# Optimization experiments

Measured on AMD Instinct MI355X. Metric: run time of the kernel, lower is better.

The kernel has to match this reference:

```python
import jax, jax.numpy as jnp
import numpy as np

B_, N, C, H = 8192, 49, 192, 6
HD = C // H
SCALE = HD ** -0.5


def setup_inputs() -> dict:
    key = jax.random.key(0)
    k0, k1, k2, k3 = jax.random.split(key, 4)
    x = jax.random.normal(k0, (B_, N, C), dtype=jnp.float32)
    mask = jax.random.randint(k1, (B_, N), 0, 2, dtype=jnp.int32)
    w_qkv = jax.random.normal(k2, (C, 3 * C), dtype=jnp.float32) * 0.02
    b_qkv = jnp.zeros((3 * C,), dtype=jnp.float32)
    w_proj = jax.random.normal(k3, (C, C), dtype=jnp.float32) * 0.02
    b_proj = jnp.zeros((C,), dtype=jnp.float32)
    return {"x": x, "mask": mask, "w_qkv": w_qkv, "b_qkv": b_qkv,
            "w_proj": w_proj, "b_proj": b_proj}


def reference(x, mask, w_qkv, b_qkv, w_proj, b_proj):
    # qkv projection: [B_, N, 3C] -> [3, B_, H, N, HD]
    qkv = (x @ w_qkv + b_qkv).reshape(B_, N, 3, H, HD).transpose(2, 0, 3, 1, 4)
    q, k, v = qkv[0], qkv[1], qkv[2]
    # scaled QK^T: [B_, H, N, N]
    attn = jnp.einsum('bhnd,bhmd->bhnm', q, k) * SCALE
    # additive key mask: mask==0 positions get -inf
    attn = jnp.where(mask[:, None, None, :] == 0, -jnp.inf, attn)
    p = jax.nn.softmax(attn, axis=-1)  # dropout p=0 -> identity
    out = jnp.einsum('bhnm,bhmd->bhnd', p, v)  # AV
    out = out.transpose(0, 2, 1, 3).reshape(B_, N, C)
    return out @ w_proj + b_proj
```

## Files before the change

### kernel.cpp

```cpp
#include <hip/hip_runtime.h>


typedef __attribute__((ext_vector_type(8))) short short8;
typedef __attribute__((ext_vector_type(4))) float f32x4;

#define SCALE 0.17677669529663687f

__device__ __forceinline__ unsigned short f2bf(float x) {
    union { float f; unsigned int i; } v; v.f = x;
    return (unsigned short)((v.i + 0x7FFFu + ((v.i >> 16) & 1u)) >> 16);
}

__device__ __forceinline__ unsigned int pkbf(float lo, float hi) {
    unsigned int r;
    asm("v_cvt_pk_bf16_f32 %0, %1, %2" : "=v"(r) : "v"(lo), "v"(hi));
    return r;
}

__device__ __forceinline__ int swz64(int row, int col) {
    return row * 64 + ((((col >> 3) ^ (row & 7)) << 3) | (col & 7));
}

__device__ __forceinline__ short8 xpose(f32x4 tlo, f32x4 thi, int srcA, bool hi) {
    unsigned int pl0 = pkbf(tlo[0], tlo[1]);
    unsigned int pl1 = pkbf(tlo[2], tlo[3]);
    unsigned int ph0 = pkbf(thi[0], thi[1]);
    unsigned int ph1 = pkbf(thi[2], thi[3]);
    unsigned int a0 = (unsigned int)__shfl((int)pl0, srcA);
    unsigned int b0 = (unsigned int)__shfl((int)ph0, srcA);
    unsigned int a1 = (unsigned int)__shfl((int)pl1, srcA);
    unsigned int b1 = (unsigned int)__shfl((int)ph1, srcA);
    unsigned int a2 = (unsigned int)__shfl((int)pl0, srcA + 16);
    unsigned int b2 = (unsigned int)__shfl((int)ph0, srcA + 16);
    unsigned int a3 = (unsigned int)__shfl((int)pl1, srcA + 16);
    unsigned int b3 = (unsigned int)__shfl((int)ph1, srcA + 16);
    union { short8 s8; unsigned int u[4]; } f;
    f.u[0] = hi ? b0 : a0;
    f.u[1] = hi ? b1 : a1;
    f.u[2] = hi ? b2 : a2;
    f.u[3] = hi ? b3 : a3;
    return f.s8;
}

__global__ void repack_kernel(const float* __restrict__ wqkv,
                              const float* __restrict__ wproj,
                              unsigned short* __restrict__ wq_pack,
                              unsigned short* __restrict__ wp_pack) {
    int idx = blockIdx.x * 256 + threadIdx.x;
    if (idx < 6 * 576 * 32) {
        int kk  = idx & 31;
        int col = (idx >> 5) % 576;
        int kt  = idx / (576 * 32);
        wq_pack[idx] = f2bf(wqkv[(kt * 32 + kk) * 576 + col]);
    } else {
        int j = idx - 6 * 576 * 32;
        if (j < 6 * 192 * 32) {
            int kk  = j & 31;
            int col = (j >> 5) % 192;
            int kt  = j / (192 * 32);
            wp_pack[j] = f2bf(wproj[(kt * 32 + kk) * 192 + col]);
        }
    }
}

__global__ __launch_bounds__(384)
void win_attn_kernel(const float* __restrict__ x,
                     const int* __restrict__ mask,
                     const float* __restrict__ bqkv,
                     const float* __restrict__ bproj,
                     const unsigned short* __restrict__ wq,
                     const unsigned short* __restrict__ wpj,
                     float* __restrict__ out) {
    __shared__ __align__(16) unsigned short region[25088];
    __shared__ __align__(16) float mbias[64];

    const int b    = blockIdx.x;
    const int tid  = threadIdx.x;
    const int lane = tid & 63;
    const int h    = tid >> 6;
    const int quad = lane >> 4;
    const int l16  = lane & 15;

    const float* xb = x + (size_t)b * 9408;
    for (int i4 = tid; i4 < 2352; i4 += 384) {
        int flat = i4 * 4;
        int n = flat / 192, c = flat % 192;
        float4 v = *(const float4*)(const void*)&xb[flat];
        uint2 pk;
        pk.x = pkbf(v.x, v.y);
        pk.y = pkbf(v.z, v.w);
        *(uint2*)(void*)&region[n * 200 + c] = pk;
    }
    if (tid < 375) {
        uint4 z = {0u, 0u, 0u, 0u};
        *(uint4*)(void*)&region[9800 + tid * 8] = z;
    }
    if (tid < 64)
        mbias[tid] = (tid < 49 && mask[b * 49 + tid] != 0) ? 0.0f : -1e30f;
    __syncthreads();

    const int  srcA = ((lane & 16) << 1) | l16;
    const bool hiq  = (lane & 32) != 0;

    int colb[6];
    #pragma unroll
    for (int t = 0; t < 6; ++t) colb[t] = (t >> 1) * 192 + h * 32 + (t & 1) * 16;

    short8 qf[4], kf[4];
    {
        f32x4 acc[4][4];
        #pragma unroll
        for (int t = 0; t < 4; ++t)
            #pragma unroll
            for (int mt = 0; mt < 4; ++mt)
                acc[t][mt] = (f32x4){0.f, 0.f, 0.f, 0.f};

        #pragma unroll
        for (int kt = 0; kt < 6; ++kt) {
            short8 af[4];
            #pragma unroll
            for (int mt = 0; mt < 4; ++mt)
                af[mt] = *(const short8*)(const void*)
                         &region[(mt * 16 + l16) * 200 + kt * 32 + quad * 8];
            #pragma unroll
            for (int t = 0; t < 4; ++t) {
                short8 bw = *(const short8*)(const void*)
                            &wq[(size_t)(kt * 576 + colb[t] + l16) * 32 + quad * 8];
                #pragma unroll
                for (int mt = 0; mt < 4; ++mt)
                    acc[t][mt] = __builtin_amdgcn_mfma_f32_16x16x32_bf16(
                                     bw, af[mt], acc[t][mt], 0, 0, 0);
            }
        }
        #pragma unroll
        for (int t = 0; t < 4; ++t) {
            f32x4 bq = *(const f32x4*)(const void*)&bqkv[colb[t] + quad * 4];
            #pragma unroll
            for (int nt = 0; nt < 4; ++nt)
                #pragma unroll
                for (int r = 0; r < 4; ++r)
                    acc[t][nt][r] += bq[r];
        }
        #pragma unroll
        for (int nt = 0; nt < 4; ++nt) {
            qf[nt] = xpose(acc[0][nt], acc[1][nt], srcA, hiq);
            kf[nt] = xpose(acc[2][nt], acc[3][nt], srcA, hiq);
        }
    }

    unsigned short* vtb = &region[12800 + h * 2048];
    {
        f32x4 accv[2][4];
        #pragma unroll
        for (int t = 0; t < 2; ++t)
            #pragma unroll
            for (int mt = 0; mt < 4; ++mt)
                accv[t][mt] = (f32x4){0.f, 0.f, 0.f, 0.f};

        #pragma unroll
        for (int kt = 0; kt < 6; ++kt) {
            short8 af[4];
            #pragma unroll
            for (int mt = 0; mt < 4; ++mt)
                af[mt] = *(const short8*)(const void*)
                         &region[(mt * 16 + l16) * 200 + kt * 32 + quad * 8];
            #pragma unroll
            for (int t = 0; t < 2; ++t) {
                short8 bw = *(const short8*)(const void*)
                            &wq[(size_t)(kt * 576 + colb[4 + t] + l16) * 32 + quad * 8];
                #pragma unroll
                for (int mt = 0; mt < 4; ++mt)
                    accv[t][mt] = __builtin_amdgcn_mfma_f32_16x16x32_bf16(
                                      af[mt], bw, accv[t][mt], 0, 0, 0);
            }
        }
        #pragma unroll
        for (int t = 0; t < 2; ++t) {
            float bv = bqkv[colb[4 + t] + l16];
            #pragma unroll
            for (int mt = 0; mt < 4; ++mt) {
                int d = t * 16 + l16;
                uint2 pk;
                pk.x = pkbf(accv[t][mt][0] + bv, accv[t][mt][1] + bv);
                pk.y = pkbf(accv[t][mt][2] + bv, accv[t][mt][3] + bv);
                *(uint2*)(void*)&vtb[swz64(d, mt * 16 + quad * 4)] = pk;
            }
        }
    }

    f32x4 mb4[4];
    #pragma unroll
    for (int mt = 0; mt < 4; ++mt)
        mb4[mt] = *(const f32x4*)(const void*)&mbias[mt * 16 + quad * 4];

    short8 ap[4][2];
    #pragma unroll
    for (int nt = 0; nt < 4; ++nt) {
        f32x4 sr[4];
        #pragma unroll
        for (int mt = 0; mt < 4; ++mt) {
            sr[mt] = (f32x4){0.f, 0.f, 0.f, 0.f};
            sr[mt] = __builtin_amdgcn_mfma_f32_16x16x32_bf16(
                         kf[mt], qf[nt], sr[mt], 0, 0, 0);
        }
        float pm[4];
        #pragma unroll
        for (int mt = 0; mt < 4; ++mt) {
            #pragma unroll
            for (int r = 0; r < 4; ++r)
                sr[mt][r] = sr[mt][r] * SCALE + mb4[mt][r];
            pm[mt] = fmaxf(fmaxf(sr[mt][0], sr[mt][1]),
                           fmaxf(sr[mt][2], sr[mt][3]));
        }
        float mx = fmaxf(fmaxf(pm[0], pm[1]), fmaxf(pm[2], pm[3]));
        mx = fmaxf(mx, __shfl_xor(mx, 16));
        mx = fmaxf(mx, __shfl_xor(mx, 32));
        float ps[4];
        #pragma unroll
        for (int mt = 0; mt < 4; ++mt) {
            #pragma unroll
            for (int r = 0; r < 4; ++r)
                sr[mt][r] = __expf(sr[mt][r] - mx);
            ps[mt] = (sr[mt][0] + sr[mt][1]) + (sr[mt][2] + sr[mt][3]);
        }
        float sum = (ps[0] + ps[1]) + (ps[2] + ps[3]);
        sum += __shfl_xor(sum, 16);
        sum += __shfl_xor(sum, 32);
        float inv = 1.0f / sum;
        #pragma unroll
        for (int mt = 0; mt < 4; ++mt)
            #pragma unroll
            for (int r = 0; r < 4; ++r)
                sr[mt][r] *= inv;
        ap[nt][0] = xpose(sr[0], sr[1], srcA, hiq);
        ap[nt][1] = xpose(sr[2], sr[3], srcA, hiq);
    }

    f32x4 o[4][2];
    #pragma unroll
    for (int mo = 0; mo < 4; ++mo)
        #pragma unroll
        for (int dt = 0; dt < 2; ++dt)
            o[mo][dt] = (f32x4){0.f, 0.f, 0.f, 0.f};

    #pragma unroll
    for (int kt = 0; kt < 2; ++kt) {
        short8 bvv[2];
        #pragma unroll
        for (int dt = 0; dt < 2; ++dt)
            bvv[dt] = *(const short8*)(const void*)
                      &vtb[swz64(dt * 16 + l16, kt * 32 + quad * 8)];
        #pragma unroll
        for (int mo = 0; mo < 4; ++mo)
            #pragma unroll
            for (int dt = 0; dt < 2; ++dt)
                o[mo][dt] = __builtin_amdgcn_mfma_f32_16x16x32_bf16(
                                ap[mo][kt], bvv[dt], o[mo][dt], 0, 0, 0);
    }

    __syncthreads();
    #pragma unroll
    for (int dt = 0; dt < 2; ++dt)
        #pragma unroll
        for (int mt = 0; mt < 4; ++mt)
            #pragma unroll
            for (int r = 0; r < 4; ++r)
                region[(mt * 16 + quad * 4 + r) * 200 + h * 32 + dt * 16 + l16]
                    = f2bf(o[mt][dt][r]);
    __syncthreads();

    f32x4 po[2][4];
    #pragma unroll
    for (int nt = 0; nt < 2; ++nt)
        #pragma unroll
        for (int mt = 0; mt < 4; ++mt)
            po[nt][mt] = (f32x4){0.f, 0.f, 0.f, 0.f};

    #pragma unroll
    for (int kt = 0; kt < 6; ++kt) {
        short8 ao[4];
        #pragma unroll
        for (int mt = 0; mt < 4; ++mt)
            ao[mt] = *(const short8*)(const void*)
                     &region[(mt * 16 + l16) * 200 + kt * 32 + quad * 8];
        #pragma unroll
        for (int nt = 0; nt < 2; ++nt) {
            int col = h * 32 + nt * 16 + l16;
            short8 bw = *(const short8*)(const void*)
                        &wpj[(size_t)(kt * 192 + col) * 32 + quad * 8];
            #pragma unroll
            for (int mt = 0; mt < 4; ++mt)
                po[nt][mt] = __builtin_amdgcn_mfma_f32_16x16x32_bf16(
                                 ao[mt], bw, po[nt][mt], 0, 0, 0);
        }
    }

    #pragma unroll
    for (int nt = 0; nt < 2; ++nt) {
        int col = h * 32 + nt * 16 + l16;
        float bv = bproj[col];
        #pragma unroll
        for (int mt = 0; mt < 4; ++mt)
            #pragma unroll
            for (int r = 0; r < 4; ++r) {
                int row = mt * 16 + quad * 4 + r;
                if (row < 49)
                    out[(size_t)b * 9408 + row * 192 + col] = po[nt][mt][r] + bv;
            }
    }
}

extern "C" void kernel_launch(void* const* d_in, const int* in_sizes, int n_in,
                              void* d_out, int out_size, void* d_ws, size_t ws_size,
                              hipStream_t stream) {
    const float* x      = (const float*)d_in[0];
    const int*   mask   = (const int*)d_in[1];
    const float* w_qkv  = (const float*)d_in[2];
    const float* b_qkv  = (const float*)d_in[3];
    const float* w_proj = (const float*)d_in[4];
    const float* b_proj = (const float*)d_in[5];
    float*       out    = (float*)d_out;

    unsigned short* wq_pack = (unsigned short*)d_ws;
    unsigned short* wp_pack = wq_pack + 110592;

    repack_kernel<<<(110592 + 36864 + 255) / 256, 256, 0, stream>>>(
        w_qkv, w_proj, wq_pack, wp_pack);
    win_attn_kernel<<<8192, 384, 0, stream>>>(x, mask, b_qkv, b_proj,
                                              wq_pack, wp_pack, out);
}
```

Before: 848.7 us.

## Make blocks persistent over eight windows with double-buffered prefetch of next window

Each block now handles eight consecutive windows instead of one. The next window's x and mask are loaded into registers at the start of each iteration and written to a second shared buffer after the attention step, so global load latency overlaps with compute. Shared memory grows (two x buffers plus per-head V tiles), and the grid shrinks from 8192 to 1024 blocks. The fewer, larger blocks may lower occupancy and weaken load balance across CUs.

```diff
diff --git a/kernel.cpp b/kernel.cpp
--- a/kernel.cpp
+++ b/kernel.cpp
@@ -5,6 +5,7 @@
 typedef __attribute__((ext_vector_type(4))) float f32x4;
 
 #define SCALE 0.17677669529663687f
+#define WPB   8
 
 __device__ __forceinline__ unsigned short f2bf(float x) {
     union { float f; unsigned int i; } v; v.f = x;
@@ -71,33 +72,16 @@
                      const unsigned short* __restrict__ wq,
                      const unsigned short* __restrict__ wpj,
                      float* __restrict__ out) {
-    __shared__ __align__(16) unsigned short region[25088];
-    __shared__ __align__(16) float mbias[64];
-
-    const int b    = blockIdx.x;
+    __shared__ __align__(16) unsigned short xbuf[2][12800];
+    __shared__ __align__(16) unsigned short vtl[6][2048];
+    __shared__ __align__(16) float mbias[2][64];
+
     const int tid  = threadIdx.x;
     const int lane = tid & 63;
     const int h    = tid >> 6;
     const int quad = lane >> 4;
     const int l16  = lane & 15;
-
-    const float* xb = x + (size_t)b * 9408;
-    for (int i4 = tid; i4 < 2352; i4 += 384) {
-        int flat = i4 * 4;
-        int n = flat / 192, c = flat % 192;
-        float4 v = *(const float4*)(const void*)&xb[flat];
-        uint2 pk;
-        pk.x = pkbf(v.x, v.y);
-        pk.y = pkbf(v.z, v.w);
-        *(uint2*)(void*)&region[n * 200 + c] = pk;
-    }
-    if (tid < 375) {
-        uint4 z = {0u, 0u, 0u, 0u};
-        *(uint4*)(void*)&region[9800 + tid * 8] = z;
-    }
-    if (tid < 64)
-        mbias[tid] = (tid < 49 && mask[b * 49 + tid] != 0) ? 0.0f : -1e30f;
-    __syncthreads();
+    const int b0   = blockIdx.x * WPB;
 
     const int  srcA = ((lane & 16) << 1) | l16;
     const bool hiq  = (lane & 32) != 0;
@@ -106,207 +90,282 @@
     #pragma unroll
     for (int t = 0; t < 6; ++t) colb[t] = (t >> 1) * 192 + h * 32 + (t & 1) * 16;
 
-    short8 qf[4], kf[4];
+    unsigned short* vtb = &vtl[h][0];
+
     {
-        f32x4 acc[4][4];
-        #pragma unroll
-        for (int t = 0; t < 4; ++t)
-            #pragma unroll
-            for (int mt = 0; mt < 4; ++mt)
-                acc[t][mt] = (f32x4){0.f, 0.f, 0.f, 0.f};
+        const float* xb = x + (size_t)b0 * 9408;
+        for (int i4 = tid; i4 < 2352; i4 += 384) {
+            int flat = i4 * 4;
+            int n = flat / 192, c = flat % 192;
+            float4 v = *(const float4*)(const void*)&xb[flat];
+            uint2 pk;
+            pk.x = pkbf(v.x, v.y);
+            pk.y = pkbf(v.z, v.w);
+            *(uint2*)(void*)&xbuf[0][n * 200 + c] = pk;
+        }
+        if (tid < 375) {
+            uint4 z = {0u, 0u, 0u, 0u};
+            *(uint4*)(void*)&xbuf[0][9800 + tid * 8] = z;
+        }
+        if (tid < 64)
+            mbias[0][tid] = (tid < 49 && mask[b0 * 49 + tid] != 0) ? 0.0f
+                                                                   : -1e30f;
+    }
+    __syncthreads();
+
+    int cur = 0;
+    for (int wi = 0; wi < WPB; ++wi, cur ^= 1) {
+        const int b = b0 + wi;
+        const bool more = (wi + 1 < WPB);
+
+        float4 st[6];
+        float4 st6 = {0.f, 0.f, 0.f, 0.f};
+        int mv = 0;
+        if (more) {
+            const float* xn = x + (size_t)(b + 1) * 9408;
+            #pragma unroll
+            for (int k = 0; k < 6; ++k)
+                st[k] = *(const float4*)(const void*)&xn[(tid + k * 384) * 4];
+            if (tid < 48)
+                st6 = *(const float4*)(const void*)&xn[(2304 + tid) * 4];
+            if (tid < 49)
+                mv = mask[(b + 1) * 49 + tid];
+        }
+
+        unsigned short* rg  = &xbuf[cur][0];
+        float*          mbp = &mbias[cur][0];
+
+        short8 qf[4], kf[4];
+        {
+            f32x4 acc[4][4];
+            #pragma unroll
+            for (int t = 0; t < 4; ++t)
+                #pragma unroll
+                for (int mt = 0; mt < 4; ++mt)
+                    acc[t][mt] = (f32x4){0.f, 0.f, 0.f, 0.f};
+
+            #pragma unroll
+            for (int kt = 0; kt < 6; ++kt) {
+                short8 af[4];
+                #pragma unroll
+                for (int mt = 0; mt < 4; ++mt)
+                    af[mt] = *(const short8*)(const void*)
+                             &rg[(mt * 16 + l16) * 200 + kt * 32 + quad * 8];
+                #pragma unroll
+                for (int t = 0; t < 4; ++t) {
+                    short8 bw = *(const short8*)(const void*)
+                                &wq[(size_t)(kt * 576 + colb[t] + l16) * 32 + quad * 8];
+                    #pragma unroll
+                    for (int mt = 0; mt < 4; ++mt)
+                        acc[t][mt] = __builtin_amdgcn_mfma_f32_16x16x32_bf16(
+                                         bw, af[mt], acc[t][mt], 0, 0, 0);
+                }
+            }
+            #pragma unroll
+            for (int t = 0; t < 4; ++t) {
+                f32x4 bq = *(const f32x4*)(const void*)&bqkv[colb[t] + quad * 4];
+                #pragma unroll
+                for (int nt = 0; nt < 4; ++nt)
+                    #pragma unroll
+                    for (int r = 0; r < 4; ++r)
+                        acc[t][nt][r] += bq[r];
+            }
+            #pragma unroll
+            for (int nt = 0; nt < 4; ++nt) {
+                qf[nt] = xpose(acc[0][nt], acc[1][nt], srcA, hiq);
+                kf[nt] = xpose(acc[2][nt], acc[3][nt], srcA, hiq);
+            }
+        }
+
+        {
+            f32x4 accv[2][4];
+            #pragma unroll
+            for (int t = 0; t < 2; ++t)
+                #pragma unroll
+                for (int mt = 0; mt < 4; ++mt)
+                    accv[t][mt] = (f32x4){0.f, 0.f, 0.f, 0.f};
+
+            #pragma unroll
+            for (int kt = 0; kt < 6; ++kt) {
+                short8 af[4];
+                #pragma unroll
+                for (int mt = 0; mt < 4; ++mt)
+                    af[mt] = *(const short8*)(const void*)
+                             &rg[(mt * 16 + l16) * 200 + kt * 32 + quad * 8];
+                #pragma unroll
+                for (int t = 0; t < 2; ++t) {
+                    short8 bw = *(const short8*)(const void*)
+                                &wq[(size_t)(kt * 576 + colb[4 + t] + l16) * 32 + quad * 8];
+                    #pragma unroll
+                    for (int mt = 0; mt < 4; ++mt)
+                        accv[t][mt] = __builtin_amdgcn_mfma_f32_16x16x32_bf16(
+                                          af[mt], bw, accv[t][mt], 0, 0, 0);
+                }
+            }
+            #pragma unroll
+            for (int t = 0; t < 2; ++t) {
+                float bv = bqkv[colb[4 + t] + l16];
+                #pragma unroll
+                for (int mt = 0; mt < 4; ++mt) {
+                    int d = t * 16 + l16;
+                    uint2 pk;
+                    pk.x = pkbf(accv[t][mt][0] + bv, accv[t][mt][1] + bv);
+                    pk.y = pkbf(accv[t][mt][2] + bv, accv[t][mt][3] + bv);
+                    *(uint2*)(void*)&vtb[swz64(d, mt * 16 + quad * 4)] = pk;
+                }
+            }
+        }
+
+        f32x4 mb4[4];
+        #pragma unroll
+        for (int mt = 0; mt < 4; ++mt)
+            mb4[mt] = *(const f32x4*)(const void*)&mbp[mt * 16 + quad * 4];
+
+        short8 ap[4][2];
+        #pragma unroll
+        for (int nt = 0; nt < 4; ++nt) {
+            f32x4 sr[4];
+            #pragma unroll
+            for (int mt = 0; mt < 4; ++mt) {
+                sr[mt] = (f32x4){0.f, 0.f, 0.f, 0.f};
+                sr[mt] = __builtin_amdgcn_mfma_f32_16x16x32_bf16(
+                             kf[mt], qf[nt], sr[mt], 0, 0, 0);
+            }
+            float pm[4];
+            #pragma unroll
+            for (int mt = 0; mt < 4; ++mt) {
+                #pragma unroll
+                for (int r = 0; r < 4; ++r)
+                    sr[mt][r] = sr[mt][r] * SCALE + mb4[mt][r];
+                pm[mt] = fmaxf(fmaxf(sr[mt][0], sr[mt][1]),
+                               fmaxf(sr[mt][2], sr[mt][3]));
+            }
+            float mx = fmaxf(fmaxf(pm[0], pm[1]), fmaxf(pm[2], pm[3]));
+            mx = fmaxf(mx, __shfl_xor(mx, 16));
+            mx = fmaxf(mx, __shfl_xor(mx, 32));
+            float ps[4];
+            #pragma unroll
+            for (int mt = 0; mt < 4; ++mt) {
+                #pragma unroll
+                for (int r = 0; r < 4; ++r)
+                    sr[mt][r] = __expf(sr[mt][r] - mx);
+                ps[mt] = (sr[mt][0] + sr[mt][1]) + (sr[mt][2] + sr[mt][3]);
+            }
+            float sum = (ps[0] + ps[1]) + (ps[2] + ps[3]);
+            sum += __shfl_xor(sum, 16);
+            sum += __shfl_xor(sum, 32);
+            float inv = 1.0f / sum;
+            #pragma unroll
+            for (int mt = 0; mt < 4; ++mt)
+                #pragma unroll
+                for (int r = 0; r < 4; ++r)
+                    sr[mt][r] *= inv;
+            ap[nt][0] = xpose(sr[0], sr[1], srcA, hiq);
+            ap[nt][1] = xpose(sr[2], sr[3], srcA, hiq);
+        }
+
+        f32x4 o[4][2];
+        #pragma unroll
+        for (int mo = 0; mo < 4; ++mo)
+            #pragma unroll
+            for (int dt = 0; dt < 2; ++dt)
+                o[mo][dt] = (f32x4){0.f, 0.f, 0.f, 0.f};
+
+        #pragma unroll
+        for (int kt = 0; kt < 2; ++kt) {
+            short8 bvv[2];
+            #pragma unroll
+            for (int dt = 0; dt < 2; ++dt)
+                bvv[dt] = *(const short8*)(const void*)
+                          &vtb[swz64(dt * 16 + l16, kt * 32 + quad * 8)];
+            #pragma unroll
+            for (int mo = 0; mo < 4; ++mo)
+                #pragma unroll
+                for (int dt = 0; dt < 2; ++dt)
+                    o[mo][dt] = __builtin_amdgcn_mfma_f32_16x16x32_bf16(
+                                    ap[mo][kt], bvv[dt], o[mo][dt], 0, 0, 0);
+        }
+
+        __syncthreads();
+
+        #pragma unroll
+        for (int dt = 0; dt < 2; ++dt)
+            #pragma unroll
+            for (int mt = 0; mt < 4; ++mt)
+                #pragma unroll
+                for (int r = 0; r < 4; ++r)
+                    rg[(mt * 16 + quad * 4 + r) * 200 + h * 32 + dt * 16 + l16]
+                        = f2bf(o[mt][dt][r]);
+
+        if (more) {
+            unsigned short* nb = &xbuf[cur ^ 1][0];
+            #pragma unroll
+            for (int k = 0; k < 6; ++k) {
+                int flat = (tid + k * 384) * 4;
+                int n = flat / 192, c = flat % 192;
+                uint2 pk;
+                pk.x = pkbf(st[k].x, st[k].y);
+                pk.y = pkbf(st[k].z, st[k].w);
+                *(uint2*)(void*)&nb[n * 200 + c] = pk;
+            }
+            if (tid < 48) {
+                int flat = (2304 + tid) * 4;
+                int n = flat / 192, c = flat % 192;
+                uint2 pk;
+                pk.x = pkbf(st6.x, st6.y);
+                pk.y = pkbf(st6.z, st6.w);
+                *(uint2*)(void*)&nb[n * 200 + c] = pk;
+            }
+            if (tid < 375) {
+                uint4 z = {0u, 0u, 0u, 0u};
+                *(uint4*)(void*)&nb[9800 + tid * 8] = z;
+            }
+            if (tid < 64)
+                mbias[cur ^ 1][tid] = (tid < 49 && mv != 0) ? 0.0f : -1e30f;
+        }
+
+        __syncthreads();
+
+        f32x4 po[2][4];
+        #pragma unroll
+        for (int nt = 0; nt < 2; ++nt)
+            #pragma unroll
+            for (int mt = 0; mt < 4; ++mt)
+                po[nt][mt] = (f32x4){0.f, 0.f, 0.f, 0.f};
 
         #pragma unroll
         for (int kt = 0; kt < 6; ++kt) {
-            short8 af[4];
-            #pragma unroll
-            for (int mt = 0; mt < 4; ++mt)
-                af[mt] = *(const short8*)(const void*)
-                         &region[(mt * 16 + l16) * 200 + kt * 32 + quad * 8];
-            #pragma unroll
-            for (int t = 0; t < 4; ++t) {
+            short8 ao[4];
+            #pragma unroll
+            for (int mt = 0; mt < 4; ++mt)
+                ao[mt] = *(const short8*)(const void*)
+                         &rg[(mt * 16 + l16) * 200 + kt * 32 + quad * 8];
+            #pragma unroll
+            for (int nt = 0; nt < 2; ++nt) {
+                int col = h * 32 + nt * 16 + l16;
                 short8 bw = *(const short8*)(const void*)
-                            &wq[(size_t)(kt * 576 + colb[t] + l16) * 32 + quad * 8];
-                #pragma unroll
-                for (int mt = 0; mt < 4; ++mt)
-                    acc[t][mt] = __builtin_amdgcn_mfma_f32_16x16x32_bf16(
-                                     bw, af[mt], acc[t][mt], 0, 0, 0);
-            }
-        }
-        #pragma unroll
-        for (int t = 0; t < 4; ++t) {
-            f32x4 bq = *(const f32x4*)(const void*)&bqkv[colb[t] + quad * 4];
-            #pragma unroll
-            for (int nt = 0; nt < 4; ++nt)
-                #pragma unroll
-                for (int r = 0; r < 4; ++r)
-                    acc[t][nt][r] += bq[r];
-        }
-        #pragma unroll
-        for (int nt = 0; nt < 4; ++nt) {
-            qf[nt] = xpose(acc[0][nt], acc[1][nt], srcA, hiq);
-            kf[nt] = xpose(acc[2][nt], acc[3][nt], srcA, hiq);
-        }
-    }
-
-    unsigned short* vtb = &region[12800 + h * 2048];
-    {
-        f32x4 accv[2][4];
-        #pragma unroll
-        for (int t = 0; t < 2; ++t)
-            #pragma unroll
-            for (int mt = 0; mt < 4; ++mt)
-                accv[t][mt] = (f32x4){0.f, 0.f, 0.f, 0.f};
-
-        #pragma unroll
-        for (int kt = 0; kt < 6; ++kt) {
-            short8 af[4];
-            #pragma unroll
-            for (int mt = 0; mt < 4; ++mt)
-                af[mt] = *(const short8*)(const void*)
-                         &region[(mt * 16 + l16) * 200 + kt * 32 + quad * 8];
-            #pragma unroll
-            for (int t = 0; t < 2; ++t) {
-                short8 bw = *(const short8*)(const void*)
-                            &wq[(size_t)(kt * 576 + colb[4 + t] + l16) * 32 + quad * 8];
-                #pragma unroll
-                for (int mt = 0; mt < 4; ++mt)
-                    accv[t][mt] = __builtin_amdgcn_mfma_f32_16x16x32_bf16(
-                                      af[mt], bw, accv[t][mt], 0, 0, 0);
-            }
-        }
-        #pragma unroll
-        for (int t = 0; t < 2; ++t) {
-            float bv = bqkv[colb[4 + t] + l16];
-            #pragma unroll
-            for (int mt = 0; mt < 4; ++mt) {
-                int d = t * 16 + l16;
-                uint2 pk;
-                pk.x = pkbf(accv[t][mt][0] + bv, accv[t][mt][1] + bv);
-                pk.y = pkbf(accv[t][mt][2] + bv, accv[t][mt][3] + bv);
-                *(uint2*)(void*)&vtb[swz64(d, mt * 16 + quad * 4)] = pk;
-            }
-        }
-    }
-
-    f32x4 mb4[4];
-    #pragma unroll
-    for (int mt = 0; mt < 4; ++mt)
-        mb4[mt] = *(const f32x4*)(const void*)&mbias[mt * 16 + quad * 4];
-
-    short8 ap[4][2];
-    #pragma unroll
-    for (int nt = 0; nt < 4; ++nt) {
-        f32x4 sr[4];
-        #pragma unroll
-        for (int mt = 0; mt < 4; ++mt) {
-            sr[mt] = (f32x4){0.f, 0.f, 0.f, 0.f};
-            sr[mt] = __builtin_amdgcn_mfma_f32_16x16x32_bf16(
-                         kf[mt], qf[nt], sr[mt], 0, 0, 0);
-        }
-        float pm[4];
-        #pragma unroll
-        for (int mt = 0; mt < 4; ++mt) {
-            #pragma unroll
-            for (int r = 0; r < 4; ++r)
-                sr[mt][r] = sr[mt][r] * SCALE + mb4[mt][r];
-            pm[mt] = fmaxf(fmaxf(sr[mt][0], sr[mt][1]),
-                           fmaxf(sr[mt][2], sr[mt][3]));
-        }
-        float mx = fmaxf(fmaxf(pm[0], pm[1]), fmaxf(pm[2], pm[3]));
-        mx = fmaxf(mx, __shfl_xor(mx, 16));
-        mx = fmaxf(mx, __shfl_xor(mx, 32));
-        float ps[4];
-        #pragma unroll
-        for (int mt = 0; mt < 4; ++mt) {
-            #pragma unroll
-            for (int r = 0; r < 4; ++r)
-                sr[mt][r] = __expf(sr[mt][r] - mx);
-            ps[mt] = (sr[mt][0] + sr[mt][1]) + (sr[mt][2] + sr[mt][3]);
-        }
-        float sum = (ps[0] + ps[1]) + (ps[2] + ps[3]);
-        sum += __shfl_xor(sum, 16);
-        sum += __shfl_xor(sum, 32);
-        float inv = 1.0f / sum;
-        #pragma unroll
-        for (int mt = 0; mt < 4; ++mt)
-            #pragma unroll
-            for (int r = 0; r < 4; ++r)
-                sr[mt][r] *= inv;
-        ap[nt][0] = xpose(sr[0], sr[1], srcA, hiq);
-        ap[nt][1] = xpose(sr[2], sr[3], srcA, hiq);
-    }
-
-    f32x4 o[4][2];
-    #pragma unroll
-    for (int mo = 0; mo < 4; ++mo)
-        #pragma unroll
-        for (int dt = 0; dt < 2; ++dt)
-            o[mo][dt] = (f32x4){0.f, 0.f, 0.f, 0.f};
-
-    #pragma unroll
-    for (int kt = 0; kt < 2; ++kt) {
-        short8 bvv[2];
-        #pragma unroll
-        for (int dt = 0; dt < 2; ++dt)
-            bvv[dt] = *(const short8*)(const void*)
-                      &vtb[swz64(dt * 16 + l16, kt * 32 + quad * 8)];
-        #pragma unroll
-        for (int mo = 0; mo < 4; ++mo)
-            #pragma unroll
-            for (int dt = 0; dt < 2; ++dt)
-                o[mo][dt] = __builtin_amdgcn_mfma_f32_16x16x32_bf16(
-                                ap[mo][kt], bvv[dt], o[mo][dt], 0, 0, 0);
-    }
-
-    __syncthreads();
-    #pragma unroll
-    for (int dt = 0; dt < 2; ++dt)
-        #pragma unroll
-        for (int mt = 0; mt < 4; ++mt)
-            #pragma unroll
-            for (int r = 0; r < 4; ++r)
-                region[(mt * 16 + quad * 4 + r) * 200 + h * 32 + dt * 16 + l16]
-                    = f2bf(o[mt][dt][r]);
-    __syncthreads();
-
-    f32x4 po[2][4];
-    #pragma unroll
-    for (int nt = 0; nt < 2; ++nt)
-        #pragma unroll
-        for (int mt = 0; mt < 4; ++mt)
-            po[nt][mt] = (f32x4){0.f, 0.f, 0.f, 0.f};
-
-    #pragma unroll
-    for (int kt = 0; kt < 6; ++kt) {
-        short8 ao[4];
-        #pragma unroll
-        for (int mt = 0; mt < 4; ++mt)
-            ao[mt] = *(const short8*)(const void*)
-                     &region[(mt * 16 + l16) * 200 + kt * 32 + quad * 8];
+                            &wpj[(size_t)(kt * 192 + col) * 32 + quad * 8];
+                #pragma unroll
+                for (int mt = 0; mt < 4; ++mt)
+                    po[nt][mt] = __builtin_amdgcn_mfma_f32_16x16x32_bf16(
+                                     ao[mt], bw, po[nt][mt], 0, 0, 0);
+            }
+        }
+
         #pragma unroll
         for (int nt = 0; nt < 2; ++nt) {
             int col = h * 32 + nt * 16 + l16;
-            short8 bw = *(const short8*)(const void*)
-                        &wpj[(size_t)(kt * 192 + col) * 32 + quad * 8];
-            #pragma unroll
-            for (int mt = 0; mt < 4; ++mt)
-                po[nt][mt] = __builtin_amdgcn_mfma_f32_16x16x32_bf16(
-                                 ao[mt], bw, po[nt][mt], 0, 0, 0);
-        }
-    }
-
-    #pragma unroll
-    for (int nt = 0; nt < 2; ++nt) {
-        int col = h * 32 + nt * 16 + l16;
-        float bv = bproj[col];
-        #pragma unroll
-        for (int mt = 0; mt < 4; ++mt)
-            #pragma unroll
-            for (int r = 0; r < 4; ++r) {
-                int row = mt * 16 + quad * 4 + r;
-                if (row < 49)
-                    out[(size_t)b * 9408 + row * 192 + col] = po[nt][mt][r] + bv;
-            }
+            float bv = bproj[col];
+            #pragma unroll
+            for (int mt = 0; mt < 4; ++mt)
+                #pragma unroll
+                for (int r = 0; r < 4; ++r) {
+                    int row = mt * 16 + quad * 4 + r;
+                    if (row < 49)
+                        out[(size_t)b * 9408 + row * 192 + col]
+                            = po[nt][mt][r] + bv;
+                }
+        }
     }
 }
 
@@ -326,6 +385,6 @@
 
     repack_kernel<<<(110592 + 36864 + 255) / 256, 256, 0, stream>>>(
         w_qkv, w_proj, wq_pack, wp_pack);
-    win_attn_kernel<<<8192, 384, 0, stream>>>(x, mask, b_qkv, b_proj,
-                                              wq_pack, wp_pack, out);
-}
+    win_attn_kernel<<<8192 / WPB, 384, 0, stream>>>(x, mask, b_qkv, b_proj,
+                                                    wq_pack, wp_pack, out);
+}
```

Result: slower. 1.370 ms (+61.4%).

## Keep V and P in MFMA registers, fuse AV into the softmax loop

Applied to the files above, without the earlier changes.

V is now kept as MFMA operand fragments in registers, converted directly from the accumulator layout, instead of being written transposed to swizzled shared memory and read back. P is converted in place with a plain pack instead of the shuffle transpose, and the AV MFMA runs per query tile inside the softmax loop. The output goes to a separate LDS region so the first barrier before writing O is dropped. Shared memory grows slightly, and correctness depends on the accumulator layout of the S^T and V tiles matching the MFMA operand layout.

```diff
diff --git a/kernel.cpp b/kernel.cpp
--- a/kernel.cpp
+++ b/kernel.cpp
@@ -17,8 +17,18 @@
     return r;
 }
 
-__device__ __forceinline__ int swz64(int row, int col) {
-    return row * 64 + ((((col >> 3) ^ (row & 7)) << 3) | (col & 7));
+__device__ __forceinline__ short8 cvt8(f32x4 lo, f32x4 hi) {
+    union { short8 s; unsigned int u[4]; } r;
+    r.u[0] = pkbf(lo[0], lo[1]);
+    r.u[1] = pkbf(lo[2], lo[3]);
+    r.u[2] = pkbf(hi[0], hi[1]);
+    r.u[3] = pkbf(hi[2], hi[3]);
+    return r.s;
+}
+
+__device__ __forceinline__ f32x4 addb(f32x4 v, float b) {
+    v[0] += b; v[1] += b; v[2] += b; v[3] += b;
+    return v;
 }
 
 __device__ __forceinline__ short8 xpose(f32x4 tlo, f32x4 thi, int srcA, bool hi) {
@@ -71,7 +81,7 @@
                      const unsigned short* __restrict__ wq,
                      const unsigned short* __restrict__ wpj,
                      float* __restrict__ out) {
-    __shared__ __align__(16) unsigned short region[25088];
+    __shared__ __align__(16) unsigned short region[25600];
     __shared__ __align__(16) float mbias[64];
 
     const int b    = blockIdx.x;
@@ -148,7 +158,7 @@
         }
     }
 
-    unsigned short* vtb = &region[12800 + h * 2048];
+    short8 vf[2][2];
     {
         f32x4 accv[2][4];
         #pragma unroll
@@ -178,13 +188,9 @@
         for (int t = 0; t < 2; ++t) {
             float bv = bqkv[colb[4 + t] + l16];
             #pragma unroll
-            for (int mt = 0; mt < 4; ++mt) {
-                int d = t * 16 + l16;
-                uint2 pk;
-                pk.x = pkbf(accv[t][mt][0] + bv, accv[t][mt][1] + bv);
-                pk.y = pkbf(accv[t][mt][2] + bv, accv[t][mt][3] + bv);
-                *(uint2*)(void*)&vtb[swz64(d, mt * 16 + quad * 4)] = pk;
-            }
+            for (int j = 0; j < 2; ++j)
+                vf[t][j] = cvt8(addb(accv[t][2 * j], bv),
+                                addb(accv[t][2 * j + 1], bv));
         }
     }
 
@@ -193,7 +199,7 @@
     for (int mt = 0; mt < 4; ++mt)
         mb4[mt] = *(const f32x4*)(const void*)&mbias[mt * 16 + quad * 4];
 
-    short8 ap[4][2];
+    unsigned short* ob = &region[12800];
     #pragma unroll
     for (int nt = 0; nt < 4; ++nt) {
         f32x4 sr[4];
@@ -232,41 +238,30 @@
             #pragma unroll
             for (int r = 0; r < 4; ++r)
                 sr[mt][r] *= inv;
-        ap[nt][0] = xpose(sr[0], sr[1], srcA, hiq);
-        ap[nt][1] = xpose(sr[2], sr[3], srcA, hiq);
-    }
-
-    f32x4 o[4][2];
-    #pragma unroll
-    for (int mo = 0; mo < 4; ++mo)
-        #pragma unroll
-        for (int dt = 0; dt < 2; ++dt)
-            o[mo][dt] = (f32x4){0.f, 0.f, 0.f, 0.f};
-
-    #pragma unroll
-    for (int kt = 0; kt < 2; ++kt) {
-        short8 bvv[2];
-        #pragma unroll
-        for (int dt = 0; dt < 2; ++dt)
-            bvv[dt] = *(const short8*)(const void*)
-                      &vtb[swz64(dt * 16 + l16, kt * 32 + quad * 8)];
-        #pragma unroll
-        for (int mo = 0; mo < 4; ++mo)
-            #pragma unroll
-            for (int dt = 0; dt < 2; ++dt)
-                o[mo][dt] = __builtin_amdgcn_mfma_f32_16x16x32_bf16(
-                                ap[mo][kt], bvv[dt], o[mo][dt], 0, 0, 0);
-    }
-
-    __syncthreads();
-    #pragma unroll
-    for (int dt = 0; dt < 2; ++dt)
-        #pragma unroll
-        for (int mt = 0; mt < 4; ++mt)
+
+        short8 pf[2];
+        pf[0] = cvt8(sr[0], sr[1]);
+        pf[1] = cvt8(sr[2], sr[3]);
+
+        f32x4 on[2];
+        #pragma unroll
+        for (int t = 0; t < 2; ++t)
+            on[t] = (f32x4){0.f, 0.f, 0.f, 0.f};
+        #pragma unroll
+        for (int j = 0; j < 2; ++j)
+            #pragma unroll
+            for (int t = 0; t < 2; ++t)
+                on[t] = __builtin_amdgcn_mfma_f32_16x16x32_bf16(
+                            pf[j], vf[t][j], on[t], 0, 0, 0);
+
+        #pragma unroll
+        for (int t = 0; t < 2; ++t)
             #pragma unroll
             for (int r = 0; r < 4; ++r)
-                region[(mt * 16 + quad * 4 + r) * 200 + h * 32 + dt * 16 + l16]
-                    = f2bf(o[mt][dt][r]);
+                ob[(nt * 16 + quad * 4 + r) * 200 + h * 32 + t * 16 + l16]
+                    = f2bf(on[t][r]);
+    }
+
     __syncthreads();
 
     f32x4 po[2][4];
@@ -282,7 +277,7 @@
         #pragma unroll
         for (int mt = 0; mt < 4; ++mt)
             ao[mt] = *(const short8*)(const void*)
-                     &region[(mt * 16 + l16) * 200 + kt * 32 + quad * 8];
+                     &ob[(mt * 16 + l16) * 200 + kt * 32 + quad * 8];
         #pragma unroll
         for (int nt = 0; nt < 2; ++nt) {
             int col = h * 32 + nt * 16 + l16;
```

Measured after the change: 834.1 us. About the same (-1.7%).
